# Kernel optimization log

Measured on AMD Instinct MI355X. Metric: run time of the kernel, lower is better.

## Reference

```python
import jax, jax.numpy as jnp
import numpy as np

B, N, M, C = 32, 4096, 512, 256  # batch, grid points, retained modes, latent channels


def setup_inputs() -> dict:
    key = jax.random.key(0)
    k1, k2 = jax.random.split(key)
    v = jax.random.normal(k1, (B, N, C), dtype=jnp.float32)
    # glorot-style scale for a (C, C) per-mode transform: std = 1/sqrt(C)
    transform_R = jax.random.normal(k2, (M, C, C), dtype=jnp.float32) * np.float32(1.0 / np.sqrt(C))
    return {"v": v, "transform_R": transform_R}


def reference(v, transform_R):
    # v: (B, N, C) real; transform_R: (M, C, C) real, applied to complex modes
    n = v.shape[1]
    m = transform_R.shape[0]
    f = jnp.fft.rfft(v, axis=1)                     # (B, N//2+1, C) complex64
    fm = f[:, :m]                                   # keep low-frequency modes (B, M, C)
    # per-mode channel mixing: out[b,m,o] = sum_i R[m,i,o] * f[b,m,i]
    gm = jnp.einsum('mio,bmi->bmo', transform_R.astype(fm.dtype), fm)
    g = jnp.zeros_like(f).at[:, :m].set(gm)         # zero-pad high modes back
    return v + jnp.fft.irfft(g, n=n, axis=1)        # residual add, (B, N, C)
```

## Files before the change

kernel.cpp:

```cpp
#include <hip/hip_runtime.h>
#include <hip/hip_fp16.h>
#include <math.h>


constexpr int BB = 32;
constexpr int CC = 256;
constexpr int MM = 512;

constexpr float PI2_4096 = 1.5339807878856412e-3f;
constexpr float PI2_512  = 1.2271846303085130e-2f;
constexpr float PI2_64   = 9.8174770424681035e-2f;
constexpr float PI_4     = 0.78539816339744831f;

typedef _Float16 f16x8 __attribute__((ext_vector_type(8)));
typedef float f32x4 __attribute__((ext_vector_type(4)));

__device__ __forceinline__ float2 cadd(float2 a, float2 b){ return make_float2(a.x+b.x, a.y+b.y); }
__device__ __forceinline__ float2 csub(float2 a, float2 b){ return make_float2(a.x-b.x, a.y-b.y); }
__device__ __forceinline__ float2 cmulf(float2 a, float2 b){ return make_float2(a.x*b.x - a.y*b.y, a.x*b.y + a.y*b.x); }

template<int S>
__device__ __forceinline__ void dif8(float2 x[8]) {
    const float R = 0.70710678118654752f;
    const float Sf = (float)S;
    float2 a0=cadd(x[0],x[4]), a1=cadd(x[1],x[5]), a2=cadd(x[2],x[6]), a3=cadd(x[3],x[7]);
    float2 d0=csub(x[0],x[4]), d1=csub(x[1],x[5]), d2=csub(x[2],x[6]), d3=csub(x[3],x[7]);
    float2 t5 = cmulf(d1, make_float2(R, -R*Sf));
    float2 t6 = make_float2(Sf*d2.y, -Sf*d2.x);
    float2 t7 = cmulf(d3, make_float2(-R, -R*Sf));
    float2 b0=cadd(a0,a2), b1=cadd(a1,a3), b2=csub(a0,a2), e3=csub(a1,a3);
    float2 b3=make_float2(Sf*e3.y, -Sf*e3.x);
    float2 b4=cadd(d0,t6), b5=cadd(t5,t7), b6=csub(d0,t6), e7=csub(t5,t7);
    float2 b7=make_float2(Sf*e7.y, -Sf*e7.x);
    x[0]=cadd(b0,b1); x[4]=csub(b0,b1);
    x[2]=cadd(b2,b3); x[6]=csub(b2,b3);
    x[1]=cadd(b4,b5); x[5]=csub(b4,b5);
    x[3]=cadd(b6,b7); x[7]=csub(b6,b7);
}

__device__ __forceinline__ void twid7(float2 x[8], float ang) {
    float s, c;
    __sincosf(ang, &s, &c);
    float2 w = make_float2(c, s), cur = w;
    x[1] = cmulf(x[1], cur);
    #pragma unroll
    for (int k = 2; k < 8; ++k) { cur = cmulf(cur, w); x[k] = cmulf(x[k], cur); }
}

__global__ __launch_bounds__(256) void k1a_kernel(const float* __restrict__ v,
                                                  __half2* __restrict__ ybuf, int b0) {
    __shared__ float2 T[64 * 65];
    const int blk = blockIdx.x;
    const int ct = blk & 1;
    const int n2 = (blk >> 1) & 63;
    const int bl = blk >> 7;
    const int bat = b0 + bl;
    const int t = threadIdx.x;
    const int p = t & 63;
    const int g = t >> 6;

    const float* vb = v + ((size_t)bat << 20) + (size_t)n2 * CC + ct * 128 + 2 * p;
    float2 X[2][8];
    #pragma unroll
    for (int s = 0; s < 2; ++s) {
        const int bd = g + 4 * s;
        #pragma unroll
        for (int a = 0; a < 8; ++a)
            X[s][a] = *(const float2*)(vb + (size_t)(8 * a + bd) * 16384);
    }
    #pragma unroll
    for (int s = 0; s < 2; ++s) {
        const int bd = g + 4 * s;
        dif8<1>(X[s]);
        twid7(X[s], -PI2_64 * (float)bd);
        float2* row = T + p * 65;
        #pragma unroll
        for (int k0 = 0; k0 < 8; ++k0) row[bd + 8 * k0] = X[s][k0];
    }
    __syncthreads();

    __half2* yb = ybuf + (size_t)bl * (64 * 64 * 128) + ct * 64 + p;
    #pragma unroll
    for (int s = 0; s < 2; ++s) {
        const int k0 = g + 4 * s;
        float2 Y[8];
        const float2* row = T + p * 65 + 8 * k0;
        #pragma unroll
        for (int b = 0; b < 8; ++b) Y[b] = row[b];
        dif8<1>(Y);
        float bs, bc, ss, sc;
        __sincosf(-PI2_4096 * (float)(n2 * k0), &bs, &bc);
        __sincosf(-PI2_512 * (float)n2, &ss, &sc);
        float2 cur = make_float2(bc, bs), stp = make_float2(sc, ss);
        #pragma unroll
        for (int k1b = 0; k1b < 8; ++k1b) {
            float2 r = cmulf(Y[k1b], cur);
            yb[(size_t)((k0 + 8 * k1b) * 64 + n2) * 128] = __floats2half2_rn(r.x, r.y);
            cur = cmulf(cur, stp);
        }
    }
}

__global__ __launch_bounds__(256) void k1b_kernel(const __half2* __restrict__ ybuf,
                                                  __half2* __restrict__ zbuf, int b0) {
    __shared__ float2 T[64 * 65];
    const int blk = blockIdx.x;
    const int ct = blk & 1;
    const int k1 = (blk >> 1) & 63;
    const int bl = blk >> 7;
    const int bat = b0 + bl;
    const int t = threadIdx.x;
    const int p = t & 63;
    const int g = t >> 6;
    const float R = 0.70710678118654752f;

    const __half2* yb = ybuf + (size_t)bl * (64 * 64 * 128) + (size_t)k1 * (64 * 128) + ct * 64 + p;
    float2 X[2][8];
    #pragma unroll
    for (int s = 0; s < 2; ++s) {
        const int bd = g + 4 * s;
        #pragma unroll
        for (int a = 0; a < 8; ++a)
            X[s][a] = __half22float2(yb[(size_t)(8 * a + bd) * 128]);
    }
    #pragma unroll
    for (int s = 0; s < 2; ++s) {
        const int bd = g + 4 * s;
        dif8<1>(X[s]);
        twid7(X[s], -PI2_64 * (float)bd);
        float2* row = T + p * 65;
        #pragma unroll
        for (int k0 = 0; k0 < 8; ++k0) row[bd + 8 * k0] = X[s][k0];
    }
    __syncthreads();

    __half2* zb = zbuf + ((size_t)(bat * 64 + k1) * 16) * 128 + ct * 64 + p;
    #pragma unroll
    for (int s = 0; s < 2; ++s) {
        const int k20 = g + 4 * s;
        float2 r[8];
        const float2* row = T + p * 65 + 8 * k20;
        #pragma unroll
        for (int b = 0; b < 8; ++b) r[b] = row[b];
        float2 sum0 = make_float2(0.f, 0.f);
        #pragma unroll
        for (int b = 0; b < 8; ++b) sum0 = cadd(sum0, r[b]);
        float2 e0 = csub(r[0], r[4]);
        float2 e1 = csub(r[1], r[5]);
        float2 e2 = csub(r[2], r[6]);
        float2 e3 = csub(r[3], r[7]);
        float2 sum7 = cadd(cadd(e0, cmulf(e1, make_float2(R, R))),
                           cadd(make_float2(-e2.y, e2.x), cmulf(e3, make_float2(-R, R))));
        zb[(size_t)k20 * 128]       = __floats2half2_rn(sum0.x, sum0.y);
        zb[(size_t)(k20 + 8) * 128] = __floats2half2_rn(sum7.x, sum7.y);
    }
}

__device__ __forceinline__ int swzh(int r, int col) {
    return r * 256 + (col ^ ((r & 7) << 3));
}

__global__ __launch_bounds__(256) void k2_kernel(const __half2* __restrict__ zbuf,
                                                 const float* __restrict__ R,
                                                 __half* __restrict__ gre,
                                                 __half* __restrict__ gim) {
    __shared__ __align__(16) __half XT[64 * 256];
    const int mh = blockIdx.x & 1;
    const int m  = blockIdx.x >> 1;
    const int t = threadIdx.x;
    const int k1 = m & 63, k2 = m >> 6;
    int k1p, jp;
    if (k1 == 0) { k1p = 0;       jp = (k2 == 0) ? 0 : (16 - k2); }
    else         { k1p = 64 - k1; jp = 15 - k2; }
    {
        const int b  = t & 31;
        const int pg = t >> 5;
        const __half2* zm = zbuf + ((size_t)(b * 64 + k1 ) * 16 + k2) * 128;
        const __half2* zp = zbuf + ((size_t)(b * 64 + k1p) * 16 + jp) * 128;
        #pragma unroll
        for (int q = 0; q < 16; ++q) {
            int pp = pg + 8 * q;
            float2 a = __half22float2(zm[pp]);
            float2 c = __half22float2(zp[pp]);
            *(__half2*)&XT[swzh(b,      2 * pp)] = __floats2half2_rn(0.5f * (a.x + c.x), 0.5f * (a.y + c.y));
            *(__half2*)&XT[swzh(b + 32, 2 * pp)] = __floats2half2_rn(0.5f * (a.y - c.y), 0.5f * (c.x - a.x));
        }
    }
    __syncthreads();

    const int w  = t >> 6;
    const int l  = t & 63;
    const int lr = l & 15;
    const int kg = l >> 4;
    const int colbase = mh * 128 + w * 32;

    f32x4 acc[4][2];
    #pragma unroll
    for (int mt = 0; mt < 4; ++mt)
        #pragma unroll
        for (int nt = 0; nt < 2; ++nt)
            acc[mt][nt] = (f32x4){0.f, 0.f, 0.f, 0.f};

    const float* Rb = R + (size_t)m * 65536 + colbase + lr;

    for (int kt = 0; kt < 8; ++kt) {
        f16x8 afrag[4];
        #pragma unroll
        for (int mt = 0; mt < 4; ++mt)
            afrag[mt] = *(const f16x8*)&XT[swzh(mt * 16 + lr, kt * 32 + kg * 8)];
        #pragma unroll
        for (int nt = 0; nt < 2; ++nt) {
            const float* rp = Rb + (size_t)(kt * 32 + kg * 8) * 256 + nt * 16;
            float rv[8];
            #pragma unroll
            for (int j = 0; j < 8; ++j) rv[j] = rp[(size_t)j * 256];
            f16x8 bhi, blo;
            #pragma unroll
            for (int j = 0; j < 8; ++j) {
                _Float16 h = (_Float16)rv[j];
                bhi[j] = h;
                blo[j] = (_Float16)(rv[j] - (float)h);
            }
            #pragma unroll
            for (int mt = 0; mt < 4; ++mt) {
                acc[mt][nt] = __builtin_amdgcn_mfma_f32_16x16x32_f16(afrag[mt], bhi, acc[mt][nt], 0, 0, 0);
                acc[mt][nt] = __builtin_amdgcn_mfma_f32_16x16x32_f16(afrag[mt], blo, acc[mt][nt], 0, 0, 0);
            }
        }
    }

    #pragma unroll
    for (int mt = 0; mt < 4; ++mt) {
        __half* plane = (mt < 2) ? gre : gim;
        const int bb = (mt & 1) * 16 + kg * 4;
        #pragma unroll
        for (int nt = 0; nt < 2; ++nt) {
            const int n = colbase + nt * 16 + lr;
            #pragma unroll
            for (int j = 0; j < 4; ++j) {
                plane[((size_t)m * BB + (bb + j)) * CC + n] = __float2half_rn(acc[mt][nt][j]);
            }
        }
    }
}

__global__ __launch_bounds__(256) void k3a_kernel(const __half* __restrict__ gre,
                                                  const __half* __restrict__ gim,
                                                  __half2* __restrict__ tbuf, int b0) {
    const int blk = blockIdx.x;
    const int ct = blk & 1;
    const int k1 = (blk >> 1) & 63;
    const int bl = blk >> 7;
    const int bat = b0 + bl;
    const int t = threadIdx.x;
    const int p = t & 63;
    const int g = t >> 6;

    float2 Zd[8], Zc[8];
    #pragma unroll
    for (int k20 = 0; k20 < 8; ++k20) {
        int m = k1 + 64 * k20;
        size_t off = ((size_t)m * BB + bat) * CC + ct * 128 + 2 * p;
        float2 a = __half22float2(*(const __half2*)(gre + off));
        float2 c = __half22float2(*(const __half2*)(gim + off));
        Zd[k20] = make_float2(a.x - c.y, c.x + a.y);
        int mp = 512 - k1 - 64 * k20;
        if (mp != 512) {
            size_t offp = ((size_t)mp * BB + bat) * CC + ct * 128 + 2 * p;
            float2 ap = __half22float2(*(const __half2*)(gre + offp));
            float2 cp = __half22float2(*(const __half2*)(gim + offp));
            Zc[k20] = make_float2(ap.x + cp.y, ap.y - cp.x);
        } else {
            Zc[k20] = make_float2(0.f, 0.f);
        }
    }

    __half2* tb = tbuf + (size_t)bl * (64 * 64 * 128) + (size_t)k1 * 128 + ct * 64 + p;
    #pragma unroll
    for (int s = 0; s < 2; ++s) {
        const int bd = g + 4 * s;
        float w8s, w8c;
        __sincosf(-PI_4 * (float)bd, &w8s, &w8c);
        float2 u[8];
        #pragma unroll
        for (int k20 = 0; k20 < 8; ++k20)
            u[k20] = cadd(Zd[k20], cmulf(Zc[k20], make_float2(w8c, w8s)));
        twid7(u, PI2_64 * (float)bd);
        dif8<-1>(u);
        float bs, bc, ss, sc;
        __sincosf(PI2_4096 * (float)(bd * k1), &bs, &bc);
        __sincosf(PI2_512 * (float)k1, &ss, &sc);
        float2 cur = make_float2(bc, bs), stp = make_float2(sc, ss);
        #pragma unroll
        for (int a = 0; a < 8; ++a) {
            float2 r = cmulf(u[a], cur);
            tb[(size_t)(8 * a + bd) * (64 * 128)] = __floats2half2_rn(r.x, r.y);
            cur = cmulf(cur, stp);
        }
    }
}

__global__ __launch_bounds__(256) void k3b_kernel(const __half2* __restrict__ tbuf,
                                                  const float* __restrict__ v,
                                                  float* __restrict__ out, int b0) {
    __shared__ float2 T[64 * 65];
    const int blk = blockIdx.x;
    const int ct = blk & 1;
    const int n2 = (blk >> 1) & 63;
    const int bl = blk >> 7;
    const int bat = b0 + bl;
    const int t = threadIdx.x;
    const int p = t & 63;
    const int g = t >> 6;

    const __half2* tb = tbuf + (size_t)bl * (64 * 64 * 128) + (size_t)n2 * (64 * 128) + ct * 64 + p;
    float2 X[2][8];
    #pragma unroll
    for (int s = 0; s < 2; ++s) {
        const int be = g + 4 * s;
        #pragma unroll
        for (int a = 0; a < 8; ++a)
            X[s][a] = __half22float2(tb[(size_t)(8 * a + be) * 128]);
    }
    #pragma unroll
    for (int s = 0; s < 2; ++s) {
        const int be = g + 4 * s;
        dif8<-1>(X[s]);
        twid7(X[s], PI2_64 * (float)be);
        float2* row = T + p * 65;
        #pragma unroll
        for (int j0 = 0; j0 < 8; ++j0) row[be + 8 * j0] = X[s][j0];
    }
    __syncthreads();

    const float sc = 1.0f / 4096.0f;
    const float* vb = v   + ((size_t)bat << 20) + (size_t)n2 * CC + ct * 128 + 2 * p;
    float*       ob = out + ((size_t)bat << 20) + (size_t)n2 * CC + ct * 128 + 2 * p;
    #pragma unroll
    for (int s = 0; s < 2; ++s) {
        const int j0 = g + 4 * s;
        float2 r[8];
        const float2* row = T + p * 65 + 8 * j0;
        #pragma unroll
        for (int b = 0; b < 8; ++b) r[b] = row[b];
        dif8<-1>(r);
        #pragma unroll
        for (int j1 = 0; j1 < 8; ++j1) {
            int n1 = j0 + 8 * j1;
            size_t off = (size_t)n1 * 16384;
            float2 vz = *(const float2*)(vb + off);
            float2 o = make_float2(vz.x + r[j1].x * sc, vz.y + r[j1].y * sc);
            *(float2*)(ob + off) = o;
        }
    }
}

extern "C" void kernel_launch(void* const* d_in, const int* in_sizes, int n_in,
                              void* d_out, int out_size, void* d_ws, size_t ws_size,
                              hipStream_t stream) {
    const float* v = (const float*)d_in[0];
    const float* R = (const float*)d_in[1];
    float* out = (float*)d_out;

    __half2* ybuf = (__half2*)d_ws;
    __half2* zbuf = ybuf + (size_t)16 * 64 * 64 * 128;
    __half*  gre  = (__half*)(zbuf + (size_t)32 * 64 * 16 * 128);
    __half*  gim  = gre + (size_t)MM * BB * CC;

    for (int h = 0; h < 2; ++h) {
        k1a_kernel<<<2048, 256, 0, stream>>>(v, ybuf, h * 16);
        k1b_kernel<<<2048, 256, 0, stream>>>(ybuf, zbuf, h * 16);
    }
    k2_kernel<<<1024, 256, 0, stream>>>(zbuf, R, gre, gim);
    for (int h = 0; h < 2; ++h) {
        k3a_kernel<<<2048, 256, 0, stream>>>(gre, gim, ybuf, h * 16);
        k3b_kernel<<<2048, 256, 0, stream>>>(ybuf, v, out, h * 16);
    }
}
```

Measured before the change: 427.7 us.

## Halve FFT shared-memory transpose tiles and double-buffer R loads in mixing GEMM

The FFT stage kernels (k1a, k1b, k3b) now run the shared-memory transpose in two halves over a 64x33 float2 tile instead of one 64x65 tile, with an extra barrier between halves. This halves LDS per block so more blocks can be resident per CU, at the cost of extra __syncthreads. In the per-mode mixing kernel (k2), the R weights for the next k-tile are prefetched into registers while the current tile's MFMAs run, hiding global load latency but using more registers.

```diff
diff --git a/kernel.cpp b/kernel.cpp
--- a/kernel.cpp
+++ b/kernel.cpp
@@ -49,7 +49,7 @@
 
 __global__ __launch_bounds__(256) void k1a_kernel(const float* __restrict__ v,
                                                   __half2* __restrict__ ybuf, int b0) {
-    __shared__ float2 T[64 * 65];
+    __shared__ float2 T[64 * 33];
     const int blk = blockIdx.x;
     const int ct = blk & 1;
     const int n2 = (blk >> 1) & 63;
@@ -73,37 +73,46 @@
         const int bd = g + 4 * s;
         dif8<1>(X[s]);
         twid7(X[s], -PI2_64 * (float)bd);
-        float2* row = T + p * 65;
-        #pragma unroll
-        for (int k0 = 0; k0 < 8; ++k0) row[bd + 8 * k0] = X[s][k0];
-    }
-    __syncthreads();
+    }
 
     __half2* yb = ybuf + (size_t)bl * (64 * 64 * 128) + ct * 64 + p;
     #pragma unroll
-    for (int s = 0; s < 2; ++s) {
-        const int k0 = g + 4 * s;
-        float2 Y[8];
-        const float2* row = T + p * 65 + 8 * k0;
-        #pragma unroll
-        for (int b = 0; b < 8; ++b) Y[b] = row[b];
-        dif8<1>(Y);
-        float bs, bc, ss, sc;
-        __sincosf(-PI2_4096 * (float)(n2 * k0), &bs, &bc);
-        __sincosf(-PI2_512 * (float)n2, &ss, &sc);
-        float2 cur = make_float2(bc, bs), stp = make_float2(sc, ss);
-        #pragma unroll
-        for (int k1b = 0; k1b < 8; ++k1b) {
-            float2 r = cmulf(Y[k1b], cur);
-            yb[(size_t)((k0 + 8 * k1b) * 64 + n2) * 128] = __floats2half2_rn(r.x, r.y);
-            cur = cmulf(cur, stp);
+    for (int h = 0; h < 2; ++h) {
+        if (h) __syncthreads();
+        {
+            float2* row = T + p * 33;
+            #pragma unroll
+            for (int s = 0; s < 2; ++s) {
+                const int bd = g + 4 * s;
+                #pragma unroll
+                for (int q = 0; q < 4; ++q) row[bd + 8 * q] = X[s][4 * h + q];
+            }
+        }
+        __syncthreads();
+        {
+            const int k0 = g + 4 * h;
+            float2 Y[8];
+            const float2* row = T + p * 33 + 8 * g;
+            #pragma unroll
+            for (int b = 0; b < 8; ++b) Y[b] = row[b];
+            dif8<1>(Y);
+            float bs, bc, ss, sc;
+            __sincosf(-PI2_4096 * (float)(n2 * k0), &bs, &bc);
+            __sincosf(-PI2_512 * (float)n2, &ss, &sc);
+            float2 cur = make_float2(bc, bs), stp = make_float2(sc, ss);
+            #pragma unroll
+            for (int k1b = 0; k1b < 8; ++k1b) {
+                float2 r = cmulf(Y[k1b], cur);
+                yb[(size_t)((k0 + 8 * k1b) * 64 + n2) * 128] = __floats2half2_rn(r.x, r.y);
+                cur = cmulf(cur, stp);
+            }
         }
     }
 }
 
 __global__ __launch_bounds__(256) void k1b_kernel(const __half2* __restrict__ ybuf,
                                                   __half2* __restrict__ zbuf, int b0) {
-    __shared__ float2 T[64 * 65];
+    __shared__ float2 T[64 * 33];
     const int blk = blockIdx.x;
     const int ct = blk & 1;
     const int k1 = (blk >> 1) & 63;
@@ -128,31 +137,40 @@
         const int bd = g + 4 * s;
         dif8<1>(X[s]);
         twid7(X[s], -PI2_64 * (float)bd);
-        float2* row = T + p * 65;
-        #pragma unroll
-        for (int k0 = 0; k0 < 8; ++k0) row[bd + 8 * k0] = X[s][k0];
-    }
-    __syncthreads();
+    }
 
     __half2* zb = zbuf + ((size_t)(bat * 64 + k1) * 16) * 128 + ct * 64 + p;
     #pragma unroll
-    for (int s = 0; s < 2; ++s) {
-        const int k20 = g + 4 * s;
-        float2 r[8];
-        const float2* row = T + p * 65 + 8 * k20;
-        #pragma unroll
-        for (int b = 0; b < 8; ++b) r[b] = row[b];
-        float2 sum0 = make_float2(0.f, 0.f);
-        #pragma unroll
-        for (int b = 0; b < 8; ++b) sum0 = cadd(sum0, r[b]);
-        float2 e0 = csub(r[0], r[4]);
-        float2 e1 = csub(r[1], r[5]);
-        float2 e2 = csub(r[2], r[6]);
-        float2 e3 = csub(r[3], r[7]);
-        float2 sum7 = cadd(cadd(e0, cmulf(e1, make_float2(R, R))),
-                           cadd(make_float2(-e2.y, e2.x), cmulf(e3, make_float2(-R, R))));
-        zb[(size_t)k20 * 128]       = __floats2half2_rn(sum0.x, sum0.y);
-        zb[(size_t)(k20 + 8) * 128] = __floats2half2_rn(sum7.x, sum7.y);
+    for (int h = 0; h < 2; ++h) {
+        if (h) __syncthreads();
+        {
+            float2* row = T + p * 33;
+            #pragma unroll
+            for (int s = 0; s < 2; ++s) {
+                const int bd = g + 4 * s;
+                #pragma unroll
+                for (int q = 0; q < 4; ++q) row[bd + 8 * q] = X[s][4 * h + q];
+            }
+        }
+        __syncthreads();
+        {
+            const int k20 = g + 4 * h;
+            float2 r[8];
+            const float2* row = T + p * 33 + 8 * g;
+            #pragma unroll
+            for (int b = 0; b < 8; ++b) r[b] = row[b];
+            float2 sum0 = make_float2(0.f, 0.f);
+            #pragma unroll
+            for (int b = 0; b < 8; ++b) sum0 = cadd(sum0, r[b]);
+            float2 e0 = csub(r[0], r[4]);
+            float2 e1 = csub(r[1], r[5]);
+            float2 e2 = csub(r[2], r[6]);
+            float2 e3 = csub(r[3], r[7]);
+            float2 sum7 = cadd(cadd(e0, cmulf(e1, make_float2(R, R))),
+                               cadd(make_float2(-e2.y, e2.x), cmulf(e3, make_float2(-R, R))));
+            zb[(size_t)k20 * 128]       = __floats2half2_rn(sum0.x, sum0.y);
+            zb[(size_t)(k20 + 8) * 128] = __floats2half2_rn(sum7.x, sum7.y);
+        }
     }
 }
 
@@ -203,23 +221,37 @@
 
     const float* Rb = R + (size_t)m * 65536 + colbase + lr;
 
+    float rv[2][16];
+    #pragma unroll
+    for (int nt = 0; nt < 2; ++nt)
+        #pragma unroll
+        for (int j = 0; j < 8; ++j)
+            rv[0][nt * 8 + j] = Rb[(size_t)(kg * 8 + j) * 256 + nt * 16];
+
+    #pragma unroll
     for (int kt = 0; kt < 8; ++kt) {
+        const int cur = kt & 1, nxt = cur ^ 1;
+        if (kt < 7) {
+            const float* rp = Rb + (size_t)((kt + 1) * 32 + kg * 8) * 256;
+            #pragma unroll
+            for (int nt = 0; nt < 2; ++nt)
+                #pragma unroll
+                for (int j = 0; j < 8; ++j)
+                    rv[nxt][nt * 8 + j] = rp[(size_t)j * 256 + nt * 16];
+        }
         f16x8 afrag[4];
         #pragma unroll
         for (int mt = 0; mt < 4; ++mt)
             afrag[mt] = *(const f16x8*)&XT[swzh(mt * 16 + lr, kt * 32 + kg * 8)];
         #pragma unroll
         for (int nt = 0; nt < 2; ++nt) {
-            const float* rp = Rb + (size_t)(kt * 32 + kg * 8) * 256 + nt * 16;
-            float rv[8];
-            #pragma unroll
-            for (int j = 0; j < 8; ++j) rv[j] = rp[(size_t)j * 256];
             f16x8 bhi, blo;
             #pragma unroll
             for (int j = 0; j < 8; ++j) {
-                _Float16 h = (_Float16)rv[j];
-                bhi[j] = h;
-                blo[j] = (_Float16)(rv[j] - (float)h);
+                float r = rv[cur][nt * 8 + j];
+                _Float16 hh = (_Float16)r;
+                bhi[j] = hh;
+                blo[j] = (_Float16)(r - (float)hh);
             }
             #pragma unroll
             for (int mt = 0; mt < 4; ++mt) {
@@ -303,7 +335,7 @@
 __global__ __launch_bounds__(256) void k3b_kernel(const __half2* __restrict__ tbuf,
                                                   const float* __restrict__ v,
                                                   float* __restrict__ out, int b0) {
-    __shared__ float2 T[64 * 65];
+    __shared__ float2 T[64 * 33];
     const int blk = blockIdx.x;
     const int ct = blk & 1;
     const int n2 = (blk >> 1) & 63;
@@ -327,30 +359,39 @@
         const int be = g + 4 * s;
         dif8<-1>(X[s]);
         twid7(X[s], PI2_64 * (float)be);
-        float2* row = T + p * 65;
-        #pragma unroll
-        for (int j0 = 0; j0 < 8; ++j0) row[be + 8 * j0] = X[s][j0];
-    }
-    __syncthreads();
+    }
 
     const float sc = 1.0f / 4096.0f;
     const float* vb = v   + ((size_t)bat << 20) + (size_t)n2 * CC + ct * 128 + 2 * p;
     float*       ob = out + ((size_t)bat << 20) + (size_t)n2 * CC + ct * 128 + 2 * p;
     #pragma unroll
-    for (int s = 0; s < 2; ++s) {
-        const int j0 = g + 4 * s;
-        float2 r[8];
-        const float2* row = T + p * 65 + 8 * j0;
-        #pragma unroll
-        for (int b = 0; b < 8; ++b) r[b] = row[b];
-        dif8<-1>(r);
-        #pragma unroll
-        for (int j1 = 0; j1 < 8; ++j1) {
-            int n1 = j0 + 8 * j1;
-            size_t off = (size_t)n1 * 16384;
-            float2 vz = *(const float2*)(vb + off);
-            float2 o = make_float2(vz.x + r[j1].x * sc, vz.y + r[j1].y * sc);
-            *(float2*)(ob + off) = o;
+    for (int h = 0; h < 2; ++h) {
+        if (h) __syncthreads();
+        {
+            float2* row = T + p * 33;
+            #pragma unroll
+            for (int s = 0; s < 2; ++s) {
+                const int be = g + 4 * s;
+                #pragma unroll
+                for (int q = 0; q < 4; ++q) row[be + 8 * q] = X[s][4 * h + q];
+            }
+        }
+        __syncthreads();
+        {
+            const int j0 = g + 4 * h;
+            float2 r[8];
+            const float2* row = T + p * 33 + 8 * g;
+            #pragma unroll
+            for (int b = 0; b < 8; ++b) r[b] = row[b];
+            dif8<-1>(r);
+            #pragma unroll
+            for (int j1 = 0; j1 < 8; ++j1) {
+                int n1 = j0 + 8 * j1;
+                size_t off = (size_t)n1 * 16384;
+                float2 vz = *(const float2*)(vb + off);
+                float2 o = make_float2(vz.x + r[j1].x * sc, vz.y + r[j1].y * sc);
+                *(float2*)(ob + off) = o;
+            }
         }
     }
 }
```

Result: no change. 432.0 us (+1.0%).
